# Performance work log

Measured on AMD Instinct MI355X. Metric: run time of the kernel, lower is better.

## Reference

```python
import jax, jax.numpy as jnp
import numpy as np

D_PAIR, C, N_HEAD = 128, 32, 4
B, N = 1, 384


def setup_inputs() -> dict:
    key = jax.random.key(0)
    ks = jax.random.split(key, 10)
    hc = N_HEAD * C
    return {
        "Z_raw": jax.random.normal(ks[0], (B, N, N, D_PAIR), jnp.float32),
        "ln_gamma": jnp.ones((D_PAIR,), jnp.float32),
        "ln_beta": jnp.zeros((D_PAIR,), jnp.float32),
        "b_weights": jax.random.normal(ks[1], (D_PAIR, N_HEAD), jnp.float32) / np.sqrt(D_PAIR),
        "Wq": jax.random.normal(ks[2], (D_PAIR, hc), jnp.float32) / np.sqrt(D_PAIR),
        "Wk": jax.random.normal(ks[3], (D_PAIR, hc), jnp.float32) / np.sqrt(D_PAIR),
        "Wv": jax.random.normal(ks[4], (D_PAIR, hc), jnp.float32) / np.sqrt(D_PAIR),
        "Wg": jax.random.normal(ks[5], (D_PAIR, hc), jnp.float32) * 0.02,
        "bg": jnp.ones((hc,), jnp.float32),  # gating bias init to 1 (gate ~ open)
        "Wo": jax.random.normal(ks[6], (hc, D_PAIR), jnp.float32) / np.sqrt(hc),
        "out_bias": jnp.zeros((D_PAIR,), jnp.float32),
    }


def reference(Z_raw, ln_gamma, ln_beta, b_weights, Wq, Wk, Wv, Wg, bg, Wo, out_bias):
    b_, n_i, n_j, d = Z_raw.shape
    h = b_weights.shape[1]
    c = Wq.shape[1] // h
    # LayerNorm over the channel dim
    mu = jnp.mean(Z_raw, axis=-1, keepdims=True)
    var = jnp.var(Z_raw, axis=-1, keepdims=True)
    Z = (Z_raw - mu) * jax.lax.rsqrt(var + 1e-5) * ln_gamma + ln_beta
    # pair bias: [B, h, q, k]
    bias = jnp.einsum('bqkc,ch->bhqk', Z, b_weights)
    # projections -> [B, I, h, J, c]
    def proj(W):
        return (Z @ W).reshape(b_, n_i, n_j, h, c).transpose(0, 1, 3, 2, 4)
    q, k, v = proj(Wq), proj(Wk), proj(Wv)
    scale = 1.0 / np.sqrt(c)
    logits = jnp.einsum('bihqc,bihkc->bihqk', q * scale, k) + bias[:, None]
    attn = jax.nn.softmax(logits, axis=-1)
    o = jnp.einsum('bihqk,bihkc->bihqc', attn, v)
    o = o.transpose(0, 1, 3, 2, 4).reshape(b_, n_i, n_j, h * c)
    gate = jax.nn.sigmoid(Z @ Wg + bg)
    out = (gate * o) @ Wo  # last_bias_fuse: no bias here
    # bias_dropout_add with row-broadcast ones mask, eval mode (no dropout scaling)
    dropout_mask = jnp.ones_like(Z_raw[:, 0:1, :, :])
    return Z_raw + (out + out_bias) * dropout_mask
```

## Files before the change

kernel.cpp:

```cpp
#include <hip/hip_runtime.h>
#include <hip/hip_bf16.h>
#include <math.h>

#define NSEQ 384
#define DPAIR 128
#define NHEAD 4
#define CDIM 32
#define KCH 128
#define VSTR 136
#define OSTR 152

typedef short bf16x8 __attribute__((ext_vector_type(8)));
typedef short bf16x4 __attribute__((ext_vector_type(4)));
typedef float f32x4 __attribute__((ext_vector_type(4)));

__device__ __forceinline__ short f2b(float f) {
    __hip_bfloat16 b = __float2bfloat16(f);
    return __builtin_bit_cast(short, b);
}
__device__ __forceinline__ float b2f(short s) {
    unsigned int u = ((unsigned int)(unsigned short)s) << 16;
    return __builtin_bit_cast(float, u);
}

__device__ __forceinline__ void mfma16(f32x4& acc, bf16x4 a, bf16x4 b) {
    asm("s_nop 1\n\tv_mfma_f32_16x16x16_bf16 %0, %1, %2, %0"
        : "+v"(acc) : "v"(a), "v"(b));
}

__global__ __launch_bounds__(256) void k_ln(
    const float* __restrict__ Zraw, const float* __restrict__ gamma,
    const float* __restrict__ beta, const float* __restrict__ bw,
    __hip_bfloat16* __restrict__ Zb, __hip_bfloat16* __restrict__ bias_perm)
{
    const int lane = threadIdx.x & 63, wave = threadIdx.x >> 6;
    const int sub = lane >> 4, l16 = lane & 15;
    const int pos = blockIdx.x * 16 + wave * 4 + sub;
    const int c0 = l16 * 8;
    const float* zp = Zraw + (size_t)pos * DPAIR + c0;
    const float4 za = *(const float4*)zp;
    const float4 zc = *(const float4*)(zp + 4);

    float s  = za.x + za.y + za.z + za.w + zc.x + zc.y + zc.z + zc.w;
    float sq = za.x*za.x + za.y*za.y + za.z*za.z + za.w*za.w
             + zc.x*zc.x + zc.y*zc.y + zc.z*zc.z + zc.w*zc.w;
#pragma unroll
    for (int o = 1; o < 16; o <<= 1) { s += __shfl_xor(s, o); sq += __shfl_xor(sq, o); }
    const float mu = s * (1.f / 128.f);
    const float rstd = rsqrtf(sq * (1.f / 128.f) - mu * mu + 1e-5f);

    const float4 ga = *(const float4*)(gamma + c0);
    const float4 gb = *(const float4*)(gamma + c0 + 4);
    const float4 ba = *(const float4*)(beta + c0);
    const float4 bb = *(const float4*)(beta + c0 + 4);
    float zn[8];
    zn[0] = (za.x - mu) * rstd * ga.x + ba.x;
    zn[1] = (za.y - mu) * rstd * ga.y + ba.y;
    zn[2] = (za.z - mu) * rstd * ga.z + ba.z;
    zn[3] = (za.w - mu) * rstd * ga.w + ba.w;
    zn[4] = (zc.x - mu) * rstd * gb.x + bb.x;
    zn[5] = (zc.y - mu) * rstd * gb.y + bb.y;
    zn[6] = (zc.z - mu) * rstd * gb.z + bb.z;
    zn[7] = (zc.w - mu) * rstd * gb.w + bb.w;

    bf16x8 hz;
#pragma unroll
    for (int k = 0; k < 8; k++) hz[k] = f2b(zn[k]);
    *(bf16x8*)((short*)Zb + (size_t)pos * DPAIR + c0) = hz;

    const float4* bw4 = (const float4*)bw;
    float4 p = {0.f, 0.f, 0.f, 0.f};
#pragma unroll
    for (int k = 0; k < 8; k++) {
        const float4 w = bw4[c0 + k];
        p.x += zn[k] * w.x; p.y += zn[k] * w.y;
        p.z += zn[k] * w.z; p.w += zn[k] * w.w;
    }
#pragma unroll
    for (int o = 1; o < 16; o <<= 1) {
        p.x += __shfl_xor(p.x, o); p.y += __shfl_xor(p.y, o);
        p.z += __shfl_xor(p.z, o); p.w += __shfl_xor(p.w, o);
    }
    if (l16 == 0) {
        const int q = pos / NSEQ, k = pos - q * NSEQ;
        const int sg = q >> 4, lrq = q & 15;
        const int c = k >> 7, kc = k & 127, t = kc >> 4, lgk = (kc >> 2) & 3, j = kc & 3;
        const size_t flat = ((size_t)(sg * 3 + c)) * 2048 + (lgk * 16 + lrq) * 32 + t * 4 + j;
        short* bp = (short*)bias_perm + flat;
        bp[0 * 147456] = f2b(p.x);
        bp[1 * 147456] = f2b(p.y);
        bp[2 * 147456] = f2b(p.z);
        bp[3 * 147456] = f2b(p.w);
    }
}

__global__ __launch_bounds__(256) void k_wt(
    const float* __restrict__ Wq, const float* __restrict__ Wk,
    const float* __restrict__ Wv, const float* __restrict__ Wg,
    const float* __restrict__ Wo, __hip_bfloat16* __restrict__ WT)
{
    const int m = blockIdx.y;
    const float* src = (m == 0) ? Wq : (m == 1) ? Wk : (m == 2) ? Wv : (m == 3) ? Wg : Wo;
    const int idx = blockIdx.x * 256 + threadIdx.x;
    const int in = idx >> 7, out = idx & 127;
    WT[m * 16384 + out * 128 + in] = __float2bfloat16(src[idx]);
}

__global__ __launch_bounds__(512, 2) void k_attn(
    const __hip_bfloat16* __restrict__ Zb,
    const __hip_bfloat16* __restrict__ WT,
    const __hip_bfloat16* __restrict__ bias_perm,
    __hip_bfloat16* __restrict__ Ob)
{
    __shared__ short Ks[KCH * 40];
    __shared__ short Vt[CDIM * VSTR];
    __shared__ short Qst[8][16 * 40];

    const int i = blockIdx.x, h = blockIdx.y;
    const int tid = threadIdx.x, wave = tid >> 6, lane = tid & 63;
    const int lr = lane & 15, lg = lane >> 4;
    const short* Zrow = (const short*)Zb + (size_t)i * NSEQ * DPAIR;
    const short* WQ = (const short*)WT + 0 * 16384 + (h * CDIM) * DPAIR;
    const short* WK = (const short*)WT + 1 * 16384 + (h * CDIM) * DPAIR;
    const short* WV = (const short*)WT + 2 * 16384 + (h * CDIM) * DPAIR;

    bf16x8 qreg[3];
    short* Qw = Qst[wave];
#pragma unroll
    for (int s = 0; s < 3; ++s) {
        const int q0 = wave * 48 + s * 16;
        f32x4 a0 = {0.f, 0.f, 0.f, 0.f}, a1 = {0.f, 0.f, 0.f, 0.f};
#pragma unroll
        for (int ks = 0; ks < 4; ks++) {
            bf16x8 afr = *(const bf16x8*)(Zrow + (q0 + lr) * DPAIR + ks * 32 + lg * 8);
            bf16x8 b0 = *(const bf16x8*)(WQ + lr * DPAIR + ks * 32 + lg * 8);
            bf16x8 b1 = *(const bf16x8*)(WQ + (16 + lr) * DPAIR + ks * 32 + lg * 8);
            a0 = __builtin_amdgcn_mfma_f32_16x16x32_bf16(afr, b0, a0, 0, 0, 0);
            a1 = __builtin_amdgcn_mfma_f32_16x16x32_bf16(afr, b1, a1, 0, 0, 0);
        }
#pragma unroll
        for (int j = 0; j < 4; j++) {
            Qw[(lg * 4 + j) * 40 + lr]      = f2b(a0[j]);
            Qw[(lg * 4 + j) * 40 + 16 + lr] = f2b(a1[j]);
        }
        asm volatile("s_waitcnt lgkmcnt(0)" ::: "memory");
        qreg[s] = *(const bf16x8*)(Qw + lr * 40 + lg * 8);
        asm volatile("" ::: "memory");
    }

    float m_run[3], l_run[3];
    f32x4 oacc[3][2];
#pragma unroll
    for (int s = 0; s < 3; s++) {
        m_run[s] = -1e30f; l_run[s] = 0.f;
        oacc[s][0] = (f32x4){0.f, 0.f, 0.f, 0.f};
        oacc[s][1] = (f32x4){0.f, 0.f, 0.f, 0.f};
    }

    const float scale = 0.17677669529663689f;

    for (int c = 0; c < 3; c++) {
        __syncthreads();
        {
            const int jt = wave;
            const int jg = c * KCH + jt * 16;
            bf16x8 afr[4];
#pragma unroll
            for (int ks = 0; ks < 4; ks++)
                afr[ks] = *(const bf16x8*)(Zrow + (jg + lr) * DPAIR + ks * 32 + lg * 8);
#pragma unroll
            for (int mat = 0; mat < 2; mat++) {
                const short* WB = mat ? WV : WK;
#pragma unroll
                for (int nt = 0; nt < 2; nt++) {
                    f32x4 acc = {0.f, 0.f, 0.f, 0.f};
#pragma unroll
                    for (int ks = 0; ks < 4; ks++) {
                        bf16x8 bfr = *(const bf16x8*)(WB + (nt * 16 + lr) * DPAIR + ks * 32 + lg * 8);
                        acc = __builtin_amdgcn_mfma_f32_16x16x32_bf16(afr[ks], bfr, acc, 0, 0, 0);
                    }
                    const int col = nt * 16 + lr;
                    if (mat == 0) {
#pragma unroll
                        for (int j = 0; j < 4; j++)
                            Ks[(jt * 16 + lg * 4 + j) * 40 + col] = f2b(acc[j]);
                    } else {
                        bf16x4 v;
#pragma unroll
                        for (int j = 0; j < 4; j++) v[j] = f2b(acc[j]);
                        *(bf16x4*)(Vt + col * VSTR + jt * 16 + lg * 4) = v;
                    }
                }
            }
        }
        __syncthreads();

#pragma unroll
        for (int s = 0; s < 3; s++) {
            const int sg = wave * 3 + s;
            const short* bbase = (const short*)bias_perm
                + ((size_t)(h * 24 + sg) * 3 + c) * 2048 + lane * 32;
            bf16x8 bv[4];
#pragma unroll
            for (int u = 0; u < 4; u++) bv[u] = *(const bf16x8*)(bbase + u * 8);

            f32x4 sacc[8];
            __builtin_amdgcn_s_setprio(1);
#pragma unroll
            for (int t = 0; t < 8; t++) {
                bf16x8 kfr = *(const bf16x8*)(Ks + (t * 16 + lr) * 40 + lg * 8);
                f32x4 z = {0.f, 0.f, 0.f, 0.f};
                sacc[t] = __builtin_amdgcn_mfma_f32_16x16x32_bf16(kfr, qreg[s], z, 0, 0, 0);
            }
            __builtin_amdgcn_s_setprio(0);

            float pm = m_run[s];
#pragma unroll
            for (int u = 0; u < 4; u++) {
#pragma unroll
                for (int t2 = 0; t2 < 2; t2++) {
                    const int t = u * 2 + t2;
#pragma unroll
                    for (int j = 0; j < 4; j++) {
                        const float v = sacc[t][j] * scale + b2f(bv[u][t2 * 4 + j]);
                        sacc[t][j] = v;
                        pm = fmaxf(pm, v);
                    }
                }
            }
            pm = fmaxf(pm, __shfl_xor(pm, 16));
            pm = fmaxf(pm, __shfl_xor(pm, 32));

            float sum = 0.f;
#pragma unroll
            for (int t = 0; t < 8; t++) {
#pragma unroll
                for (int j = 0; j < 4; j++) {
                    const float p = __expf(sacc[t][j] - pm);
                    sacc[t][j] = p;
                    sum += p;
                }
            }
            sum += __shfl_xor(sum, 16);
            sum += __shfl_xor(sum, 32);

            const float fs = __expf(m_run[s] - pm);
            l_run[s] = l_run[s] * fs + sum;
            m_run[s] = pm;
            oacc[s][0] *= fs;
            oacc[s][1] *= fs;

            bf16x4 pf[8];
#pragma unroll
            for (int t = 0; t < 8; t++) {
                bf16x4 v;
                v[0] = f2b(sacc[t][0]); v[1] = f2b(sacc[t][1]);
                v[2] = f2b(sacc[t][2]); v[3] = f2b(sacc[t][3]);
                pf[t] = v;
            }

            __builtin_amdgcn_s_setprio(1);
#pragma unroll
            for (int t = 0; t < 8; t++) {
                bf16x4 v0 = *(const bf16x4*)(Vt + lr * VSTR + t * 16 + lg * 4);
                bf16x4 v1 = *(const bf16x4*)(Vt + (16 + lr) * VSTR + t * 16 + lg * 4);
                mfma16(oacc[s][0], v0, pf[t]);
                mfma16(oacc[s][1], v1, pf[t]);
            }
            __builtin_amdgcn_s_setprio(0);
        }
    }

    asm volatile("s_nop 7\n\ts_nop 7" ::: "memory");

#pragma unroll
    for (int s = 0; s < 3; s++) {
        const int q0 = wave * 48 + s * 16;
        const float invl = 1.f / l_run[s];
        const size_t row = (size_t)i * NSEQ + q0 + lr;
#pragma unroll
        for (int nt = 0; nt < 2; nt++) {
            bf16x4 o;
#pragma unroll
            for (int j = 0; j < 4; j++) o[j] = f2b(oacc[s][nt][j] * invl);
            *(bf16x4*)((short*)Ob + row * DPAIR + h * CDIM + nt * 16 + lg * 4) = o;
        }
    }
}

__global__ __launch_bounds__(256) void k_out(
    const float* __restrict__ Zraw,
    const __hip_bfloat16* __restrict__ Zb,
    const __hip_bfloat16* __restrict__ Ob,
    const __hip_bfloat16* __restrict__ WT,
    const float* __restrict__ bg,
    const float* __restrict__ out_bias,
    float* __restrict__ out)
{
    __shared__ short Zt[64 * OSTR];
    __shared__ short Ot[64 * OSTR];
    __shared__ short GOt[64 * OSTR];
    const int pos0 = blockIdx.x * 64;
    const int tid = threadIdx.x, wave = tid >> 6, lane = tid & 63;
    const int lr = lane & 15, lg = lane >> 4;

#pragma unroll
    for (int it = 0; it < 4; ++it) {
        const int cidx = tid + 256 * it;
        const int row = cidx >> 4, cc = (cidx & 15) * 8;
        *(bf16x8*)(Zt + row * OSTR + cc) =
            *(const bf16x8*)((const short*)Zb + (size_t)(pos0 + row) * DPAIR + cc);
        *(bf16x8*)(Ot + row * OSTR + cc) =
            *(const bf16x8*)((const short*)Ob + (size_t)(pos0 + row) * DPAIR + cc);
    }
    __syncthreads();

    const short* WgT = (const short*)WT + 3 * 16384;
    const short* WoT = (const short*)WT + 4 * 16384;
    const int m0 = wave * 16;

    bf16x8 afr[4];
#pragma unroll
    for (int ks = 0; ks < 4; ks++)
        afr[ks] = *(const bf16x8*)(Zt + (m0 + lr) * OSTR + ks * 32 + lg * 8);
#pragma unroll
    for (int nt = 0; nt < 8; nt++) {
        f32x4 acc = {0.f, 0.f, 0.f, 0.f};
#pragma unroll
        for (int ks = 0; ks < 4; ks++) {
            bf16x8 bfr = *(const bf16x8*)(WgT + (nt * 16 + lr) * DPAIR + ks * 32 + lg * 8);
            acc = __builtin_amdgcn_mfma_f32_16x16x32_bf16(afr[ks], bfr, acc, 0, 0, 0);
        }
        const int col = nt * 16 + lr;
        const float bgv = bg[col];
#pragma unroll
        for (int j = 0; j < 4; j++) {
            const int row = m0 + lg * 4 + j;
            const float g = 1.f / (1.f + __expf(-(acc[j] + bgv)));
            const float ov = b2f(Ot[row * OSTR + col]);
            GOt[row * OSTR + col] = f2b(g * ov);
        }
    }
    __syncthreads();

#pragma unroll
    for (int ks = 0; ks < 4; ks++)
        afr[ks] = *(const bf16x8*)(GOt + (m0 + lr) * OSTR + ks * 32 + lg * 8);
#pragma unroll
    for (int nt = 0; nt < 8; nt++) {
        f32x4 acc = {0.f, 0.f, 0.f, 0.f};
#pragma unroll
        for (int ks = 0; ks < 4; ks++) {
            bf16x8 bfr = *(const bf16x8*)(WoT + (nt * 16 + lr) * DPAIR + ks * 32 + lg * 8);
            acc = __builtin_amdgcn_mfma_f32_16x16x32_bf16(afr[ks], bfr, acc, 0, 0, 0);
        }
        const int col = nt * 16 + lr;
        const float ob = out_bias[col];
#pragma unroll
        for (int j = 0; j < 4; j++) {
            const size_t idx = (size_t)(pos0 + m0 + lg * 4 + j) * DPAIR + col;
            out[idx] = Zraw[idx] + acc[j] + ob;
        }
    }
}

extern "C" void kernel_launch(void* const* d_in, const int* in_sizes, int n_in,
                              void* d_out, int out_size, void* d_ws, size_t ws_size,
                              hipStream_t stream)
{
    const float* Zraw     = (const float*)d_in[0];
    const float* gamma    = (const float*)d_in[1];
    const float* beta     = (const float*)d_in[2];
    const float* bw       = (const float*)d_in[3];
    const float* Wq       = (const float*)d_in[4];
    const float* Wk       = (const float*)d_in[5];
    const float* Wv       = (const float*)d_in[6];
    const float* Wg       = (const float*)d_in[7];
    const float* bg       = (const float*)d_in[8];
    const float* Wo       = (const float*)d_in[9];
    const float* out_bias = (const float*)d_in[10];

    char* ws = (char*)d_ws;
    const size_t zbytes = (size_t)NSEQ * NSEQ * DPAIR * 2;
    __hip_bfloat16* Zb        = (__hip_bfloat16*)ws;
    __hip_bfloat16* Ob        = (__hip_bfloat16*)(ws + zbytes);
    __hip_bfloat16* bias_perm = (__hip_bfloat16*)(ws + 2 * zbytes);
    __hip_bfloat16* WT        = (__hip_bfloat16*)(ws + 2 * zbytes + (size_t)NHEAD * NSEQ * NSEQ * 2);

    k_ln<<<NSEQ * NSEQ / 16, 256, 0, stream>>>(Zraw, gamma, beta, bw, Zb, bias_perm);
    k_wt<<<dim3(64, 5), 256, 0, stream>>>(Wq, Wk, Wv, Wg, Wo, WT);
    k_attn<<<dim3(NSEQ, NHEAD), 512, 0, stream>>>(Zb, WT, bias_perm, Ob);
    k_out<<<NSEQ * NSEQ / 64, 256, 0, stream>>>(Zraw, Zb, Ob, WT, bg, out_bias, (float*)d_out);
}
```

Baseline: 291.6 us.

## Double-buffer K/V projection tiles to overlap next chunk with attention

K and V tiles in shared memory are now double-buffered: the projection for the next key chunk is computed before the attention math on the current chunk, with one barrier per chunk instead of two. This is meant to let projection MFMAs and global loads overlap with the softmax and PV work and to cut barrier stalls. The max and sum reductions are split into independent partials for more instruction-level parallelism, and the V row stride changes to alter LDS bank mapping. The cost is twice the LDS for K/V, which may reduce occupancy under the 512-thread, 2-blocks launch bound, plus more register pressure.

After: 328.9 us. +12.8%, slower.

```diff
diff --git a/kernel.cpp b/kernel.cpp
--- a/kernel.cpp
+++ b/kernel.cpp
@@ -7,7 +7,7 @@
 #define NHEAD 4
 #define CDIM 32
 #define KCH 128
-#define VSTR 136
+#define VSTR 140
 #define OSTR 152
 
 typedef short bf16x8 __attribute__((ext_vector_type(8)));
@@ -112,8 +112,8 @@
     const __hip_bfloat16* __restrict__ bias_perm,
     __hip_bfloat16* __restrict__ Ob)
 {
-    __shared__ short Ks[KCH * 40];
-    __shared__ short Vt[CDIM * VSTR];
+    __shared__ short Ks[2][KCH * 40];
+    __shared__ short Vt[2][CDIM * VSTR];
     __shared__ short Qst[8][16 * 40];
 
     const int i = blockIdx.x, h = blockIdx.y;
@@ -124,6 +124,39 @@
     const short* WK = (const short*)WT + 1 * 16384 + (h * CDIM) * DPAIR;
     const short* WV = (const short*)WT + 2 * 16384 + (h * CDIM) * DPAIR;
 
+    auto proj = [&](int c, short* KsC, short* VtC) {
+        const int jt = wave;
+        const int jg = c * KCH + jt * 16;
+        bf16x8 afr[4];
+#pragma unroll
+        for (int ks = 0; ks < 4; ks++)
+            afr[ks] = *(const bf16x8*)(Zrow + (jg + lr) * DPAIR + ks * 32 + lg * 8);
+#pragma unroll
+        for (int mat = 0; mat < 2; mat++) {
+            const short* WB = mat ? WV : WK;
+#pragma unroll
+            for (int nt = 0; nt < 2; nt++) {
+                f32x4 acc = {0.f, 0.f, 0.f, 0.f};
+#pragma unroll
+                for (int ks = 0; ks < 4; ks++) {
+                    bf16x8 bfr = *(const bf16x8*)(WB + (nt * 16 + lr) * DPAIR + ks * 32 + lg * 8);
+                    acc = __builtin_amdgcn_mfma_f32_16x16x32_bf16(afr[ks], bfr, acc, 0, 0, 0);
+                }
+                const int col = nt * 16 + lr;
+                if (mat == 0) {
+#pragma unroll
+                    for (int j = 0; j < 4; j++)
+                        KsC[(jt * 16 + lg * 4 + j) * 40 + col] = f2b(acc[j]);
+                } else {
+                    bf16x4 v;
+#pragma unroll
+                    for (int j = 0; j < 4; j++) v[j] = f2b(acc[j]);
+                    *(bf16x4*)(VtC + col * VSTR + jt * 16 + lg * 4) = v;
+                }
+            }
+        }
+    };
+
     bf16x8 qreg[3];
     short* Qw = Qst[wave];
 #pragma unroll
@@ -159,41 +192,16 @@
 
     const float scale = 0.17677669529663689f;
 
+    proj(0, Ks[0], Vt[0]);
+    __syncthreads();
+
+#pragma unroll
     for (int c = 0; c < 3; c++) {
-        __syncthreads();
-        {
-            const int jt = wave;
-            const int jg = c * KCH + jt * 16;
-            bf16x8 afr[4];
-#pragma unroll
-            for (int ks = 0; ks < 4; ks++)
-                afr[ks] = *(const bf16x8*)(Zrow + (jg + lr) * DPAIR + ks * 32 + lg * 8);
-#pragma unroll
-            for (int mat = 0; mat < 2; mat++) {
-                const short* WB = mat ? WV : WK;
-#pragma unroll
-                for (int nt = 0; nt < 2; nt++) {
-                    f32x4 acc = {0.f, 0.f, 0.f, 0.f};
-#pragma unroll
-                    for (int ks = 0; ks < 4; ks++) {
-                        bf16x8 bfr = *(const bf16x8*)(WB + (nt * 16 + lr) * DPAIR + ks * 32 + lg * 8);
-                        acc = __builtin_amdgcn_mfma_f32_16x16x32_bf16(afr[ks], bfr, acc, 0, 0, 0);
-                    }
-                    const int col = nt * 16 + lr;
-                    if (mat == 0) {
-#pragma unroll
-                        for (int j = 0; j < 4; j++)
-                            Ks[(jt * 16 + lg * 4 + j) * 40 + col] = f2b(acc[j]);
-                    } else {
-                        bf16x4 v;
-#pragma unroll
-                        for (int j = 0; j < 4; j++) v[j] = f2b(acc[j]);
-                        *(bf16x4*)(Vt + col * VSTR + jt * 16 + lg * 4) = v;
-                    }
-                }
-            }
-        }
-        __syncthreads();
+        const int cur = c & 1;
+        if (c < 2) proj(c + 1, Ks[cur ^ 1], Vt[cur ^ 1]);
+
+        const short* KsC = Ks[cur];
+        const short* VtC = Vt[cur];
 
 #pragma unroll
         for (int s = 0; s < 3; s++) {
@@ -208,39 +216,43 @@
             __builtin_amdgcn_s_setprio(1);
 #pragma unroll
             for (int t = 0; t < 8; t++) {
-                bf16x8 kfr = *(const bf16x8*)(Ks + (t * 16 + lr) * 40 + lg * 8);
+                bf16x8 kfr = *(const bf16x8*)(KsC + (t * 16 + lr) * 40 + lg * 8);
                 f32x4 z = {0.f, 0.f, 0.f, 0.f};
                 sacc[t] = __builtin_amdgcn_mfma_f32_16x16x32_bf16(kfr, qreg[s], z, 0, 0, 0);
             }
             __builtin_amdgcn_s_setprio(0);
 
-            float pm = m_run[s];
+            float vmax[8];
 #pragma unroll
             for (int u = 0; u < 4; u++) {
 #pragma unroll
                 for (int t2 = 0; t2 < 2; t2++) {
                     const int t = u * 2 + t2;
-#pragma unroll
-                    for (int j = 0; j < 4; j++) {
-                        const float v = sacc[t][j] * scale + b2f(bv[u][t2 * 4 + j]);
-                        sacc[t][j] = v;
-                        pm = fmaxf(pm, v);
-                    }
+                    float v0 = sacc[t][0] * scale + b2f(bv[u][t2 * 4 + 0]);
+                    float v1 = sacc[t][1] * scale + b2f(bv[u][t2 * 4 + 1]);
+                    float v2 = sacc[t][2] * scale + b2f(bv[u][t2 * 4 + 2]);
+                    float v3 = sacc[t][3] * scale + b2f(bv[u][t2 * 4 + 3]);
+                    sacc[t][0] = v0; sacc[t][1] = v1; sacc[t][2] = v2; sacc[t][3] = v3;
+                    vmax[t] = fmaxf(fmaxf(v0, v1), fmaxf(v2, v3));
                 }
             }
+            float m01 = fmaxf(vmax[0], vmax[1]), m23 = fmaxf(vmax[2], vmax[3]);
+            float m45 = fmaxf(vmax[4], vmax[5]), m67 = fmaxf(vmax[6], vmax[7]);
+            float pm = fmaxf(fmaxf(fmaxf(m01, m23), fmaxf(m45, m67)), m_run[s]);
             pm = fmaxf(pm, __shfl_xor(pm, 16));
             pm = fmaxf(pm, __shfl_xor(pm, 32));
 
-            float sum = 0.f;
+            float su0 = 0.f, su1 = 0.f, su2 = 0.f, su3 = 0.f;
 #pragma unroll
             for (int t = 0; t < 8; t++) {
-#pragma unroll
-                for (int j = 0; j < 4; j++) {
-                    const float p = __expf(sacc[t][j] - pm);
-                    sacc[t][j] = p;
-                    sum += p;
-                }
+                const float p0 = __expf(sacc[t][0] - pm);
+                const float p1 = __expf(sacc[t][1] - pm);
+                const float p2 = __expf(sacc[t][2] - pm);
+                const float p3 = __expf(sacc[t][3] - pm);
+                sacc[t][0] = p0; sacc[t][1] = p1; sacc[t][2] = p2; sacc[t][3] = p3;
+                su0 += p0; su1 += p1; su2 += p2; su3 += p3;
             }
+            float sum = (su0 + su1) + (su2 + su3);
             sum += __shfl_xor(sum, 16);
             sum += __shfl_xor(sum, 32);
 
@@ -250,25 +262,20 @@
             oacc[s][0] *= fs;
             oacc[s][1] *= fs;
 
-            bf16x4 pf[8];
+            __builtin_amdgcn_s_setprio(1);
 #pragma unroll
             for (int t = 0; t < 8; t++) {
-                bf16x4 v;
-                v[0] = f2b(sacc[t][0]); v[1] = f2b(sacc[t][1]);
-                v[2] = f2b(sacc[t][2]); v[3] = f2b(sacc[t][3]);
-                pf[t] = v;
-            }
-
-            __builtin_amdgcn_s_setprio(1);
-#pragma unroll
-            for (int t = 0; t < 8; t++) {
-                bf16x4 v0 = *(const bf16x4*)(Vt + lr * VSTR + t * 16 + lg * 4);
-                bf16x4 v1 = *(const bf16x4*)(Vt + (16 + lr) * VSTR + t * 16 + lg * 4);
-                mfma16(oacc[s][0], v0, pf[t]);
-                mfma16(oacc[s][1], v1, pf[t]);
+                bf16x4 pf;
+                pf[0] = f2b(sacc[t][0]); pf[1] = f2b(sacc[t][1]);
+                pf[2] = f2b(sacc[t][2]); pf[3] = f2b(sacc[t][3]);
+                bf16x4 v0 = *(const bf16x4*)(VtC + lr * VSTR + t * 16 + lg * 4);
+                bf16x4 v1 = *(const bf16x4*)(VtC + (16 + lr) * VSTR + t * 16 + lg * 4);
+                mfma16(oacc[s][0], v0, pf);
+                mfma16(oacc[s][1], v1, pf);
             }
             __builtin_amdgcn_s_setprio(0);
         }
+        __syncthreads();
     }
 
     asm volatile("s_nop 7\n\ts_nop 7" ::: "memory");
```
